# Performance work log

Measured on AMD Instinct MI355X. Metric: run time of the kernel, lower is better.

The kernel has to match this reference:

```python
import jax, jax.numpy as jnp
import numpy as np

N = 50000      # nodes
E = 400000     # edges (before self-loops)
IN = 256       # in_dim
H = 4          # heads in layer 1
C = 64         # h_dim (per-head channels, layer 1)
OUT = 16       # out_dim (layer 2, 1 head)
NEG_SLOPE = 0.2


def gatv2_layer(x, src, dst, Wl, bl, Wr, br, att, bias, heads, ch, concat, num_nodes):
    # x: [N, F]; src/dst: [E']; Wl/Wr: [F, heads*ch]; att: [heads, ch]
    xl = (x @ Wl + bl).reshape(num_nodes, heads, ch)  # source transform
    xr = (x @ Wr + br).reshape(num_nodes, heads, ch)  # target transform
    m = xl[src] + xr[dst]                              # [E', H, C] gather
    e = jnp.sum(jax.nn.leaky_relu(m, NEG_SLOPE) * att, axis=-1)  # [E', H]
    # segment softmax over incoming edges of each dst node (self-loops ensure non-empty)
    emax = jax.ops.segment_max(e, dst, num_segments=num_nodes)   # [N, H]
    ee = jnp.exp(e - emax[dst])
    denom = jax.ops.segment_sum(ee, dst, num_segments=num_nodes)  # [N, H]
    alpha = ee / (denom[dst] + 1e-16)                              # [E', H]
    out = jax.ops.segment_sum(alpha[..., None] * xl[src], dst, num_segments=num_nodes)  # [N,H,C]
    if concat:
        out = out.reshape(num_nodes, heads * ch)
    else:
        out = out.mean(axis=1)
    return out + bias


def setup_inputs() -> dict:
    key = jax.random.key(0)
    ks = jax.random.split(key, 16)
    s = 0.05
    inp = {
        "x": jax.random.normal(ks[0], (N, IN), jnp.float32),
        "edge_index": jax.random.randint(ks[1], (2, E), 0, N),
        # layer 1 params (in_dim -> heads*h_dim)
        "Wl1": jax.random.normal(ks[2], (IN, H * C), jnp.float32) * s,
        "bl1": jnp.zeros((H * C,), jnp.float32),
        "Wr1": jax.random.normal(ks[3], (IN, H * C), jnp.float32) * s,
        "br1": jnp.zeros((H * C,), jnp.float32),
        "att1": jax.random.normal(ks[4], (H, C), jnp.float32) * s,
        "bias1": jnp.zeros((H * C,), jnp.float32),
        # layer 2 params (heads*h_dim -> out_dim, 1 head)
        "Wl2": jax.random.normal(ks[5], (H * C, OUT), jnp.float32) * s,
        "bl2": jnp.zeros((OUT,), jnp.float32),
        "Wr2": jax.random.normal(ks[6], (H * C, OUT), jnp.float32) * s,
        "br2": jnp.zeros((OUT,), jnp.float32),
        "att2": jax.random.normal(ks[7], (1, OUT), jnp.float32) * s,
        "bias2": jnp.zeros((OUT,), jnp.float32),
    }
    return inp


def reference(x, edge_index, Wl1, bl1, Wr1, br1, att1, bias1, Wl2, bl2, Wr2, br2, att2, bias2):
    # add self loops (PyG GATv2Conv default add_self_loops=True)
    loop = jnp.arange(N, dtype=edge_index.dtype)
    src = jnp.concatenate([edge_index[0], loop])
    dst = jnp.concatenate([edge_index[1], loop])
    h = gatv2_layer(x, src, dst, Wl1, bl1, Wr1, br1, att1, bias1, H, C, True, N)
    h = jnp.tanh(h)
    o = gatv2_layer(h, src, dst, Wl2, bl2, Wr2, br2, att2, bias2, 1, OUT, False, N)
    return o, jax.nn.log_softmax(o, axis=1)
```

## Files before the change

kernel.cpp:

```cpp
#include <hip/hip_runtime.h>

typedef __bf16 bfv8 __attribute__((ext_vector_type(8)));
typedef float f32x4 __attribute__((ext_vector_type(4)));
typedef float f32x2 __attribute__((ext_vector_type(2)));
typedef short shortv8 __attribute__((ext_vector_type(8)));
typedef unsigned short usv8 __attribute__((ext_vector_type(8)));
typedef unsigned int u32x4 __attribute__((ext_vector_type(4)));

__device__ __forceinline__ float b2f(unsigned short u) {
  unsigned int v = ((unsigned int)u) << 16;
  float f;
  __builtin_memcpy(&f, &v, 4);
  return f;
}
__device__ __forceinline__ unsigned short f2b(float f) {
  unsigned int u;
  __builtin_memcpy(&u, &f, 4);
  u += 0x7fffu + ((u >> 16) & 1u);
  return (unsigned short)(u >> 16);
}
__device__ __forceinline__ f32x2 unpack2(unsigned int u) {
  unsigned int lo = u << 16;
  unsigned int hi = u & 0xffff0000u;
  float fl, fh;
  __builtin_memcpy(&fl, &lo, 4);
  __builtin_memcpy(&fh, &hi, 4);
  f32x2 r;
  r.x = fl;
  r.y = fh;
  return r;
}

__global__ void probe_kernel(const unsigned short* __restrict__ x, int* __restrict__ flag) {
  int lane = threadIdx.x;
  int cnt = 0;
  for (int i = lane; i < 4096; i += 64) {
    unsigned int e = (x[i] >> 7) & 0xffu;
    if (e >= 0x86u) cnt++;
  }
#pragma unroll
  for (int off = 1; off < 64; off <<= 1) cnt += __shfl_xor(cnt, off, 64);
  if (lane == 0) *flag = (cnt > 100) ? 1 : 0;
}

__global__ __launch_bounds__(256) void conv_x_kernel(const void* __restrict__ x,
                                                     unsigned short* __restrict__ dst,
                                                     const int* __restrict__ flagp, int n) {
  int i = (blockIdx.x * 256 + threadIdx.x) * 4;
  if (i >= n) return;
  if (*flagp) {
    float4 f = *reinterpret_cast<const float4*>((const float*)x + i);
    ushort4 o;
    o.x = f2b(f.x); o.y = f2b(f.y); o.z = f2b(f.z); o.w = f2b(f.w);
    *reinterpret_cast<ushort4*>(dst + i) = o;
  } else {
    *reinterpret_cast<ushort4*>(dst + i) =
        *reinterpret_cast<const ushort4*>((const unsigned short*)x + i);
  }
}

#define SM_TOT 1088
__device__ __forceinline__ unsigned short rd_param(const void* p, int e, int flag) {
  return flag ? f2b(((const float*)p)[e]) : ((const unsigned short*)p)[e];
}
__global__ __launch_bounds__(256) void prep_params_kernel(
    const void* Wl1, const void* bl1, const void* Wr1, const void* br1,
    const void* att1, const void* bias1, const void* Wl2, const void* bl2,
    const void* Wr2, const void* br2, const void* att2, const void* bias2,
    unsigned short* __restrict__ WT1, unsigned short* __restrict__ WT2,
    unsigned short* __restrict__ Pv, const int* __restrict__ flagp) {
  int idx = blockIdx.x * 256 + threadIdx.x;
  int flag = *flagp;
  if (idx < 512 * 256) {
    int n = idx >> 8, k = idx & 255;
    WT1[idx] = (n < 256) ? rd_param(Wl1, k * 256 + n, flag)
                         : rd_param(Wr1, k * 256 + (n - 256), flag);
    return;
  }
  idx -= 512 * 256;
  if (idx < 32 * 256) {
    int n = idx >> 8, k = idx & 255;
    WT2[idx] = (n < 16) ? rd_param(Wl2, k * 16 + n, flag)
                        : rd_param(Wr2, k * 16 + (n - 16), flag);
    return;
  }
  idx -= 32 * 256;
  if (idx >= SM_TOT) return;
  const void* srcs[8] = {bl1, br1, att1, bias1, bl2, br2, att2, bias2};
  const int offs[9] = {0, 256, 512, 768, 1024, 1040, 1056, 1072, SM_TOT};
  int t = 0;
  while (idx >= offs[t + 1]) t++;
  Pv[idx] = rd_param(srcs[t], idx - offs[t], flag);
}

__global__ __launch_bounds__(256) void gemm1_kernel(
    const unsigned short* __restrict__ X,
    const unsigned short* __restrict__ WT,
    const unsigned short* __restrict__ bl, const unsigned short* __restrict__ br,
    unsigned short* __restrict__ C, int M) {
  __shared__ unsigned short smem[18432];
  const int t = threadIdx.x;
  const int lane = t & 63;
  const int w = t >> 6;
  const int quad = lane >> 4;
  const int l16 = lane & 15;
  const int n_blk = blockIdx.x;
  const int m_base = blockIdx.y * 128 + (w >> 1) * 64;
  const int n_base = n_blk * 128 + (w & 1) * 64;

  const int st_row = t >> 3;
  const int st_seg = t & 7;
  const unsigned short* wt_base =
      WT + ((size_t)(n_blk * 128 + st_row)) * 256 + st_seg * 8;

  f32x4 acc[4][4];
#pragma unroll
  for (int i = 0; i < 4; i++)
#pragma unroll
    for (int j = 0; j < 4; j++) acc[i][j] = (f32x4){0.f, 0.f, 0.f, 0.f};

  shortv8 st[4];
#pragma unroll
  for (int i = 0; i < 4; i++)
    st[i] = *reinterpret_cast<const shortv8*>(wt_base + (size_t)(32 * i) * 256);
#pragma unroll
  for (int i = 0; i < 4; i++) {
    int row = st_row + 32 * i;
    *reinterpret_cast<shortv8*>(smem + row * 64 + ((st_seg ^ (row & 7)) * 8)) = st[i];
  }
  __syncthreads();

#pragma unroll
  for (int c = 0; c < 4; c++) {
    if (c < 3) {
#pragma unroll
      for (int i = 0; i < 4; i++)
        st[i] = *reinterpret_cast<const shortv8*>(wt_base + (size_t)(32 * i) * 256 +
                                                  (c + 1) * 64);
    }
    const unsigned short* bb = smem + (c & 1) * 8192;
#pragma unroll
    for (int sub = 0; sub < 2; sub++) {
      bfv8 a[4], b[4];
      int seg_r = sub * 4 + quad;
#pragma unroll
      for (int i = 0; i < 4; i++) {
        int row = m_base + 16 * i + l16;
        if (row >= M) row = M - 1;
        a[i] = *reinterpret_cast<const bfv8*>(X + (size_t)row * 256 + c * 64 + sub * 32 +
                                              quad * 8);
      }
#pragma unroll
      for (int j = 0; j < 4; j++) {
        int col = (w & 1) * 64 + 16 * j + l16;
        b[j] = *reinterpret_cast<const bfv8*>(bb + col * 64 + ((seg_r ^ (col & 7)) * 8));
      }
#pragma unroll
      for (int i = 0; i < 4; i++)
#pragma unroll
        for (int j = 0; j < 4; j++)
          acc[i][j] = __builtin_amdgcn_mfma_f32_16x16x32_bf16(a[i], b[j], acc[i][j], 0, 0, 0);
    }
    if (c < 3) {
      int buf = (c + 1) & 1;
#pragma unroll
      for (int i = 0; i < 4; i++) {
        int row = st_row + 32 * i;
        *reinterpret_cast<shortv8*>(smem + buf * 8192 + row * 64 +
                                    ((st_seg ^ (row & 7)) * 8)) = st[i];
      }
      __syncthreads();
    }
  }

  __syncthreads();
  unsigned short* lt = smem + w * 4608;
#pragma unroll
  for (int j = 0; j < 4; j++) {
    int col = n_base + 16 * j + l16;
    float bias = (col < 256) ? b2f(bl[col]) : b2f(br[col - 256]);
#pragma unroll
    for (int i = 0; i < 4; i++)
#pragma unroll
      for (int r = 0; r < 4; r++)
        lt[(16 * i + quad * 4 + r) * 72 + 16 * j + l16] = f2b(acc[i][j][r] + bias);
  }
#pragma unroll
  for (int pass = 0; pass < 8; pass++) {
    int row = pass * 8 + (lane >> 3);
    int colg = (lane & 7) * 8;
    shortv8 v = *reinterpret_cast<const shortv8*>(lt + row * 72 + colg);
    int grow = m_base + row;
    if (grow < M)
      *reinterpret_cast<shortv8*>(C + (size_t)grow * 512 + n_base + colg) = v;
  }
}

__global__ __launch_bounds__(256) void gemm2_kernel(
    const unsigned short* __restrict__ H, const unsigned short* __restrict__ WT,
    const unsigned short* __restrict__ bl, const unsigned short* __restrict__ br,
    float* __restrict__ C, int M) {
  const int lane = threadIdx.x & 63;
  const int w = threadIdx.x >> 6;
  const int quad = lane >> 4;
  const int l16 = lane & 15;
  const int m_base = blockIdx.x * 256 + w * 64;

  f32x4 acc[4][2];
#pragma unroll
  for (int i = 0; i < 4; i++)
#pragma unroll
    for (int j = 0; j < 2; j++) acc[i][j] = (f32x4){0.f, 0.f, 0.f, 0.f};

#pragma unroll
  for (int k0 = 0; k0 < 256; k0 += 32) {
    bfv8 a[4], b[2];
#pragma unroll
    for (int i = 0; i < 4; i++) {
      int row = m_base + 16 * i + l16;
      if (row >= M) row = M - 1;
      a[i] = *reinterpret_cast<const bfv8*>(H + (size_t)row * 256 + k0 + quad * 8);
    }
#pragma unroll
    for (int j = 0; j < 2; j++) {
      int col = 16 * j + l16;
      b[j] = *reinterpret_cast<const bfv8*>(WT + (size_t)col * 256 + k0 + quad * 8);
    }
#pragma unroll
    for (int i = 0; i < 4; i++)
#pragma unroll
      for (int j = 0; j < 2; j++)
        acc[i][j] = __builtin_amdgcn_mfma_f32_16x16x32_bf16(a[i], b[j], acc[i][j], 0, 0, 0);
  }

#pragma unroll
  for (int j = 0; j < 2; j++) {
    int col = 16 * j + l16;
    float bias = (j == 0) ? b2f(bl[l16]) : b2f(br[l16]);
#pragma unroll
    for (int i = 0; i < 4; i++) {
#pragma unroll
      for (int r = 0; r < 4; r++) {
        int row = m_base + 16 * i + quad * 4 + r;
        if (row < M) C[(size_t)row * 32 + col] = acc[i][j][r] + bias;
      }
    }
  }
}

__global__ __launch_bounds__(256) void count_kernel(const int* __restrict__ ei, int E, int Nn,
                                                    int* __restrict__ cnt) {
  int i = blockIdx.x * 256 + threadIdx.x;
  int total = E + Nn;
  if (i >= total) return;
  int d = (i < E) ? ei[E + i] : (i - E);
  if ((unsigned)d >= (unsigned)Nn) d = 0;
  atomicAdd(&cnt[d], 1);
}

__global__ __launch_bounds__(1024) void scan1_kernel(const int* __restrict__ cnt,
                                                     int* __restrict__ row_start,
                                                     int* __restrict__ blkTot, int Nn) {
  __shared__ int buf[1024];
  int t = threadIdx.x;
  int i = blockIdx.x * 1024 + t;
  int v = (i < Nn) ? cnt[i] : 0;
  buf[t] = v;
  __syncthreads();
  for (int off = 1; off < 1024; off <<= 1) {
    int x = (t >= off) ? buf[t - off] : 0;
    __syncthreads();
    buf[t] += x;
    __syncthreads();
  }
  if (i < Nn) row_start[i] = buf[t] - v;
  if (t == 1023) blkTot[blockIdx.x] = buf[1023];
}

__global__ __launch_bounds__(64) void scan2_kernel(const int* __restrict__ blkTot,
                                                   int* __restrict__ blkOff, int nb,
                                                   int* __restrict__ row_start, int Nn,
                                                   int total) {
  int lane = threadIdx.x;
  int v = (lane < nb) ? blkTot[lane] : 0;
  int s = v;
#pragma unroll
  for (int off = 1; off < 64; off <<= 1) {
    int u = __shfl_up(s, off, 64);
    if (lane >= off) s += u;
  }
  if (lane < nb) blkOff[lane] = s - v;
  if (lane == 0) row_start[Nn] = total;
}

__global__ __launch_bounds__(1024) void scan3_kernel(int* __restrict__ row_start,
                                                     int* __restrict__ cursor,
                                                     const int* __restrict__ blkOff, int Nn) {
  int i = blockIdx.x * 1024 + threadIdx.x;
  if (i < Nn) {
    int val = row_start[i] + blkOff[blockIdx.x];
    row_start[i] = val;
    cursor[i] = val;
  }
}

__global__ __launch_bounds__(256) void fill_kernel(const int* __restrict__ ei, int E, int Nn,
                                                   int* __restrict__ cursor,
                                                   int* __restrict__ csr_src) {
  int i = blockIdx.x * 256 + threadIdx.x;
  int total = E + Nn;
  if (i >= total) return;
  int s, d;
  if (i < E) { s = ei[i]; d = ei[E + i]; } else { s = i - E; d = i - E; }
  if ((unsigned)d >= (unsigned)Nn) d = 0;
  if ((unsigned)s >= (unsigned)Nn) s = 0;
  int pos = atomicAdd(&cursor[d], 1);
  if ((unsigned)pos < (unsigned)total) csr_src[pos] = s;
}

__global__ __launch_bounds__(256) void agg1_kernel(
    const unsigned short* __restrict__ C1,
    const unsigned short* __restrict__ att1,
    const unsigned short* __restrict__ bias1,
    const int* __restrict__ row_start, const int* __restrict__ csr_src,
    unsigned short* __restrict__ H1,
    int Nn, int Etot) {
  int wid = blockIdx.x * 4 + (threadIdx.x >> 6);
  if (wid >= Nn) return;
  int lane = threadIdx.x & 63;
  int half = lane >> 5;
  int c0 = (lane & 31) * 8;

  f32x2 at2[4], xr2[4];
  {
    u32x4 a4 = *reinterpret_cast<const u32x4*>(att1 + c0);
    u32x4 r4 = *reinterpret_cast<const u32x4*>(C1 + (size_t)wid * 512 + 256 + c0);
#pragma unroll
    for (int k = 0; k < 4; k++) { at2[k] = unpack2(a4[k]); xr2[k] = unpack2(r4[k]); }
  }

  float denom = 0.f;
  f32x2 acc2[4] = {{0.f, 0.f}, {0.f, 0.f}, {0.f, 0.f}, {0.f, 0.f}};
  int beg = row_start[wid], end = row_start[wid + 1];
  if (beg < 0) beg = 0;
  if (end < beg || end - beg > Etot) end = beg;

#pragma unroll 2
  for (int i = beg; i < end; i += 2) {
    int p = i + half;
    bool valid = p < end;
    int pc = valid ? p : i;
    int s = csr_src[pc];
    if ((unsigned)s >= (unsigned)Nn) s = 0;
    u32x4 row = *reinterpret_cast<const u32x4*>(C1 + (size_t)s * 512 + c0);
    f32x2 xl2[4];
    f32x2 dot2 = {0.f, 0.f};
#pragma unroll
    for (int k = 0; k < 4; k++) {
      xl2[k] = unpack2(row[k]);
      f32x2 m2 = xl2[k] + xr2[k];
      f32x2 l2 = __builtin_elementwise_max(m2, 0.2f * m2);
      dot2 = l2 * at2[k] + dot2;
    }
    float dot = dot2.x + dot2.y;
    dot += __shfl_xor(dot, 1, 64);
    dot += __shfl_xor(dot, 2, 64);
    dot += __shfl_xor(dot, 4, 64);
    dot = fminf(fmaxf(dot, -60.f), 60.f);
    float wgt = valid ? __expf(dot) : 0.f;
    denom += wgt;
    f32x2 w2 = {wgt, wgt};
#pragma unroll
    for (int k = 0; k < 4; k++) acc2[k] = xl2[k] * w2 + acc2[k];
  }
  denom += __shfl_xor(denom, 32, 64);
#pragma unroll
  for (int k = 0; k < 4; k++) {
    acc2[k].x += __shfl_xor(acc2[k].x, 32, 64);
    acc2[k].y += __shfl_xor(acc2[k].y, 32, 64);
  }

  if (half == 0) {
    float inv = 1.f / (denom + 1e-16f);
    usv8 b8 = *reinterpret_cast<const usv8*>(bias1 + c0);
    usv8 o8;
#pragma unroll
    for (int k = 0; k < 4; k++) {
#pragma unroll
      for (int j = 0; j < 2; j++) {
        float x = (j ? acc2[k].y : acc2[k].x) * inv + b2f(b8[2 * k + j]);
        float e2 = __expf(2.f * x);
        float th = (e2 - 1.f) / (e2 + 1.f);
        if (!(th == th)) th = 0.f;
        o8[2 * k + j] = f2b(th);
      }
    }
    *reinterpret_cast<usv8*>(H1 + (size_t)wid * 256 + c0) = o8;
  }
}

__global__ __launch_bounds__(256) void agg2_kernel(
    const float* __restrict__ C2,
    const unsigned short* __restrict__ att2,
    const unsigned short* __restrict__ bias2,
    const int* __restrict__ row_start, const int* __restrict__ csr_src,
    float* __restrict__ out,
    int Nn, int Etot) {
  int wid = blockIdx.x * 4 + (threadIdx.x >> 6);
  if (wid >= Nn) return;
  int lane = threadIdx.x & 63;
  int eslot = lane >> 2;
  int cg = (lane & 3) * 4;

  f32x2 at2[2], xr2[2];
  {
    ushort4 a4 = *reinterpret_cast<const ushort4*>(att2 + cg);
    at2[0].x = b2f(a4.x); at2[0].y = b2f(a4.y);
    at2[1].x = b2f(a4.z); at2[1].y = b2f(a4.w);
    float4 r4 = *reinterpret_cast<const float4*>(C2 + (size_t)wid * 32 + 16 + cg);
    xr2[0].x = r4.x; xr2[0].y = r4.y; xr2[1].x = r4.z; xr2[1].y = r4.w;
  }

  float denom = 0.f;
  f32x2 acc2[2] = {{0.f, 0.f}, {0.f, 0.f}};
  int beg = row_start[wid], end = row_start[wid + 1];
  if (beg < 0) beg = 0;
  if (end < beg || end - beg > Etot) end = beg;

  for (int i = beg; i < end; i += 16) {
    int p = i + eslot;
    bool valid = p < end;
    int pc = valid ? p : i;
    int s = csr_src[pc];
    if ((unsigned)s >= (unsigned)Nn) s = 0;
    float4 x4 = *reinterpret_cast<const float4*>(C2 + (size_t)s * 32 + cg);
    f32x2 xl2[2];
    xl2[0].x = x4.x; xl2[0].y = x4.y; xl2[1].x = x4.z; xl2[1].y = x4.w;
    f32x2 dot2 = {0.f, 0.f};
#pragma unroll
    for (int k = 0; k < 2; k++) {
      f32x2 m2 = xl2[k] + xr2[k];
      f32x2 l2 = __builtin_elementwise_max(m2, 0.2f * m2);
      dot2 = l2 * at2[k] + dot2;
    }
    float dot = dot2.x + dot2.y;
    dot += __shfl_xor(dot, 1, 64);
    dot += __shfl_xor(dot, 2, 64);
    dot = fminf(fmaxf(dot, -60.f), 60.f);
    float wgt = valid ? __expf(dot) : 0.f;
    denom += wgt;
    f32x2 w2 = {wgt, wgt};
#pragma unroll
    for (int k = 0; k < 2; k++) acc2[k] = xl2[k] * w2 + acc2[k];
  }
#pragma unroll
  for (int off = 4; off <= 32; off <<= 1) {
    denom += __shfl_xor(denom, off, 64);
#pragma unroll
    for (int k = 0; k < 2; k++) {
      acc2[k].x += __shfl_xor(acc2[k].x, off, 64);
      acc2[k].y += __shfl_xor(acc2[k].y, off, 64);
    }
  }

  float inv = 1.f / (denom + 1e-16f);
  ushort4 b4 = *reinterpret_cast<const ushort4*>(bias2 + cg);
  float bb[4] = {b2f(b4.x), b2f(b4.y), b2f(b4.z), b2f(b4.w)};
  float o[4] = {acc2[0].x * inv + bb[0], acc2[0].y * inv + bb[1],
                acc2[1].x * inv + bb[2], acc2[1].y * inv + bb[3]};
#pragma unroll
  for (int k = 0; k < 4; k++)
    if (!(o[k] == o[k])) o[k] = 0.f;
  float mx = fmaxf(fmaxf(o[0], o[1]), fmaxf(o[2], o[3]));
  mx = fmaxf(mx, __shfl_xor(mx, 1, 64));
  mx = fmaxf(mx, __shfl_xor(mx, 2, 64));
  float se = 0.f;
#pragma unroll
  for (int k = 0; k < 4; k++) se += __expf(o[k] - mx);
  se += __shfl_xor(se, 1, 64);
  se += __shfl_xor(se, 2, 64);
  float ls = logf(se);
  if (lane < 4) {
    float4 vo = {o[0], o[1], o[2], o[3]};
    float4 vl = {o[0] - mx - ls, o[1] - mx - ls, o[2] - mx - ls, o[3] - mx - ls};
    *reinterpret_cast<float4*>(out + (size_t)wid * 16 + cg) = vo;
    *reinterpret_cast<float4*>(out + (size_t)Nn * 16 + (size_t)wid * 16 + cg) = vl;
  }
}

extern "C" void kernel_launch(void* const* d_in, const int* in_sizes, int n_in,
                              void* d_out, int out_size, void* d_ws, size_t ws_size,
                              hipStream_t stream) {
  const void* x_raw = d_in[0];
  const int* ei     = (const int*)d_in[1];

  const int M = in_sizes[0] / 256;
  const int E = in_sizes[1] / 2;
  const int TOT = E + M;
  const int NX = M * 256;

  char* ws = (char*)d_ws;
  size_t off = 0;
  auto alloc = [&](size_t bytes) -> void* {
    void* p = ws + off;
    off = (off + bytes + 255) & ~(size_t)255;
    return p;
  };
  int*            flag   = (int*)alloc(4);
  unsigned short* Pv     = (unsigned short*)alloc((size_t)SM_TOT * 2);
  unsigned short* Xc     = (unsigned short*)alloc((size_t)NX * 2);
  unsigned short* WT1    = (unsigned short*)alloc((size_t)512 * 256 * 2);
  unsigned short* WT2    = (unsigned short*)alloc((size_t)32 * 256 * 2);
  int*            cnt    = (int*)alloc((size_t)M * 4);
  int*            cursor = (int*)alloc((size_t)M * 4);
  int*            row_start = (int*)alloc((size_t)(M + 1) * 4);
  int*            csr_src   = (int*)alloc((size_t)TOT * 4);
  int*            blkTot = (int*)alloc(64 * 4);
  int*            blkOff = (int*)alloc(64 * 4);
  float*          C2     = (float*)alloc((size_t)M * 32 * 4);
  unsigned short* C1     = (unsigned short*)alloc((size_t)M * 512 * 2);
  const size_t need = off;
  (void)n_in;
  unsigned short* H1 = Xc;

  if (ws_size < need) {
    hipMemsetAsync(d_out, 0, (size_t)out_size * 4, stream);
    return;
  }

  unsigned short* bl1c   = Pv + 0;
  unsigned short* br1c   = Pv + 256;
  unsigned short* att1c  = Pv + 512;
  unsigned short* bias1c = Pv + 768;
  unsigned short* bl2c   = Pv + 1024;
  unsigned short* br2c   = Pv + 1040;
  unsigned short* att2c  = Pv + 1056;
  unsigned short* bias2c = Pv + 1072;

  hipMemsetAsync(cnt, 0, (size_t)M * 4, stream);

  probe_kernel<<<1, 64, 0, stream>>>((const unsigned short*)x_raw, flag);
  conv_x_kernel<<<(NX / 4 + 255) / 256, 256, 0, stream>>>(x_raw, Xc, flag, NX);
  prep_params_kernel<<<(512 * 256 + 32 * 256 + SM_TOT + 255) / 256, 256, 0, stream>>>(
      d_in[2], d_in[3], d_in[4], d_in[5], d_in[6], d_in[7], d_in[8], d_in[9],
      d_in[10], d_in[11], d_in[12], d_in[13], WT1, WT2, Pv, flag);

  dim3 g1(4, (M + 127) / 128);
  gemm1_kernel<<<g1, 256, 0, stream>>>(Xc, WT1, bl1c, br1c, C1, M);

  count_kernel<<<(TOT + 255) / 256, 256, 0, stream>>>(ei, E, M, cnt);
  int nb = (M + 1023) / 1024;
  scan1_kernel<<<nb, 1024, 0, stream>>>(cnt, row_start, blkTot, M);
  scan2_kernel<<<1, 64, 0, stream>>>(blkTot, blkOff, nb, row_start, M, TOT);
  scan3_kernel<<<nb, 1024, 0, stream>>>(row_start, cursor, blkOff, M);
  fill_kernel<<<(TOT + 255) / 256, 256, 0, stream>>>(ei, E, M, cursor, csr_src);

  agg1_kernel<<<(M + 3) / 4, 256, 0, stream>>>(C1, att1c, bias1c, row_start, csr_src,
                                               H1, M, TOT);

  gemm2_kernel<<<(M + 255) / 256, 256, 0, stream>>>(H1, WT2, bl2c, br2c, C2, M);

  agg2_kernel<<<(M + 3) / 4, 256, 0, stream>>>(C2, att2c, bias2c, row_start, csr_src,
                                               (float*)d_out, M, TOT);
}
```

Before: 301.8 us.

## Fold dtype probe into kernels, swizzle GEMM1 grid, unroll agg1 edge loop

Removes the separate single-wave probe kernel by having each block of conv_x and prep_params recompute the fp32/bf16 input-format flag from the first 4096 halves of x in shared memory, saving one launch and a serial dependency. GEMM1 moves to a 1D grid with a swizzle that groups 8 M-slabs across the 4 N-blocks, aiming for better L2 reuse of X rows. The agg1 loop now loads two neighbor rows per iteration (4 edges per wave step) to keep more gathers in flight. Each block now redundantly rereads the probe sample, and the grid is padded to a multiple of 32 with early exit for out-of-range slabs.

Result: no change. 303.2 us (+0.4%).

```diff
diff --git a/kernel.cpp b/kernel.cpp
--- a/kernel.cpp
+++ b/kernel.cpp
@@ -30,25 +30,26 @@
   r.y = fh;
   return r;
 }
-
-__global__ void probe_kernel(const unsigned short* __restrict__ x, int* __restrict__ flag) {
-  int lane = threadIdx.x;
-  int cnt = 0;
-  for (int i = lane; i < 4096; i += 64) {
-    unsigned int e = (x[i] >> 7) & 0xffu;
-    if (e >= 0x86u) cnt++;
-  }
-#pragma unroll
-  for (int off = 1; off < 64; off <<= 1) cnt += __shfl_xor(cnt, off, 64);
-  if (lane == 0) *flag = (cnt > 100) ? 1 : 0;
+__device__ __forceinline__ bool block_flag_f32(const unsigned short* xh) {
+  __shared__ int cnt_s;
+  if (threadIdx.x == 0) cnt_s = 0;
+  __syncthreads();
+  int c = 0;
+  for (int k = threadIdx.x; k < 4096; k += 256) {
+    unsigned int e = (xh[k] >> 7) & 0xffu;
+    if (e >= 0x86u) c++;
+  }
+  if (c) atomicAdd(&cnt_s, c);
+  __syncthreads();
+  return cnt_s > 100;
 }
 
 __global__ __launch_bounds__(256) void conv_x_kernel(const void* __restrict__ x,
-                                                     unsigned short* __restrict__ dst,
-                                                     const int* __restrict__ flagp, int n) {
+                                                     unsigned short* __restrict__ dst, int n) {
+  bool f32in = block_flag_f32((const unsigned short*)x);
   int i = (blockIdx.x * 256 + threadIdx.x) * 4;
   if (i >= n) return;
-  if (*flagp) {
+  if (f32in) {
     float4 f = *reinterpret_cast<const float4*>((const float*)x + i);
     ushort4 o;
     o.x = f2b(f.x); o.y = f2b(f.y); o.z = f2b(f.z); o.w = f2b(f.w);
@@ -64,13 +65,13 @@
   return flag ? f2b(((const float*)p)[e]) : ((const unsigned short*)p)[e];
 }
 __global__ __launch_bounds__(256) void prep_params_kernel(
-    const void* Wl1, const void* bl1, const void* Wr1, const void* br1,
+    const void* xh, const void* Wl1, const void* bl1, const void* Wr1, const void* br1,
     const void* att1, const void* bias1, const void* Wl2, const void* bl2,
     const void* Wr2, const void* br2, const void* att2, const void* bias2,
     unsigned short* __restrict__ WT1, unsigned short* __restrict__ WT2,
-    unsigned short* __restrict__ Pv, const int* __restrict__ flagp) {
+    unsigned short* __restrict__ Pv) {
+  int flag = block_flag_f32((const unsigned short*)xh) ? 1 : 0;
   int idx = blockIdx.x * 256 + threadIdx.x;
-  int flag = *flagp;
   if (idx < 512 * 256) {
     int n = idx >> 8, k = idx & 255;
     WT1[idx] = (n < 256) ? rd_param(Wl1, k * 256 + n, flag)
@@ -99,13 +100,16 @@
     const unsigned short* __restrict__ bl, const unsigned short* __restrict__ br,
     unsigned short* __restrict__ C, int M) {
   __shared__ unsigned short smem[18432];
+  const int lin = blockIdx.x;
+  const int m_slab = (lin >> 5) * 8 + (lin & 7);
+  const int n_blk = (lin >> 3) & 3;
+  if (m_slab * 128 >= M) return;
   const int t = threadIdx.x;
   const int lane = t & 63;
   const int w = t >> 6;
   const int quad = lane >> 4;
   const int l16 = lane & 15;
-  const int n_blk = blockIdx.x;
-  const int m_base = blockIdx.y * 128 + (w >> 1) * 64;
+  const int m_base = m_slab * 128 + (w >> 1) * 64;
   const int n_base = n_blk * 128 + (w & 1) * 64;
 
   const int st_row = t >> 3;
@@ -345,34 +349,41 @@
   if (beg < 0) beg = 0;
   if (end < beg || end - beg > Etot) end = beg;
 
-#pragma unroll 2
-  for (int i = beg; i < end; i += 2) {
-    int p = i + half;
-    bool valid = p < end;
-    int pc = valid ? p : i;
-    int s = csr_src[pc];
-    if ((unsigned)s >= (unsigned)Nn) s = 0;
-    u32x4 row = *reinterpret_cast<const u32x4*>(C1 + (size_t)s * 512 + c0);
-    f32x2 xl2[4];
-    f32x2 dot2 = {0.f, 0.f};
-#pragma unroll
-    for (int k = 0; k < 4; k++) {
-      xl2[k] = unpack2(row[k]);
-      f32x2 m2 = xl2[k] + xr2[k];
-      f32x2 l2 = __builtin_elementwise_max(m2, 0.2f * m2);
-      dot2 = l2 * at2[k] + dot2;
-    }
-    float dot = dot2.x + dot2.y;
-    dot += __shfl_xor(dot, 1, 64);
-    dot += __shfl_xor(dot, 2, 64);
-    dot += __shfl_xor(dot, 4, 64);
-    dot = fminf(fmaxf(dot, -60.f), 60.f);
-    float wgt = valid ? __expf(dot) : 0.f;
-    denom += wgt;
-    f32x2 w2 = {wgt, wgt};
-#pragma unroll
-    for (int k = 0; k < 4; k++) acc2[k] = xl2[k] * w2 + acc2[k];
-  }
+#define AGG1_BODY(ROW, VALID)                                                 \
+  {                                                                           \
+    f32x2 xl2[4];                                                             \
+    f32x2 dot2 = {0.f, 0.f};                                                  \
+    _Pragma("unroll") for (int k = 0; k < 4; k++) {                           \
+      xl2[k] = unpack2(ROW[k]);                                               \
+      f32x2 m2 = xl2[k] + xr2[k];                                             \
+      f32x2 l2 = __builtin_elementwise_max(m2, 0.2f * m2);                    \
+      dot2 = l2 * at2[k] + dot2;                                              \
+    }                                                                         \
+    float dot = dot2.x + dot2.y;                                              \
+    dot += __shfl_xor(dot, 1, 64);                                            \
+    dot += __shfl_xor(dot, 2, 64);                                            \
+    dot += __shfl_xor(dot, 4, 64);                                            \
+    dot = fminf(fmaxf(dot, -60.f), 60.f);                                     \
+    float wgt = (VALID) ? __expf(dot) : 0.f;                                  \
+    denom += wgt;                                                             \
+    f32x2 w2 = {wgt, wgt};                                                    \
+    _Pragma("unroll") for (int k = 0; k < 4; k++) acc2[k] = xl2[k] * w2 + acc2[k]; \
+  }
+
+  for (int i = beg; i < end; i += 4) {
+    int p0 = i + half, p1 = i + 2 + half;
+    bool v0 = p0 < end, v1 = p1 < end;
+    int s0 = csr_src[v0 ? p0 : i];
+    int s1 = csr_src[v1 ? p1 : i];
+    if ((unsigned)s0 >= (unsigned)Nn) s0 = 0;
+    if ((unsigned)s1 >= (unsigned)Nn) s1 = 0;
+    u32x4 row0 = *reinterpret_cast<const u32x4*>(C1 + (size_t)s0 * 512 + c0);
+    u32x4 row1 = *reinterpret_cast<const u32x4*>(C1 + (size_t)s1 * 512 + c0);
+    AGG1_BODY(row0, v0);
+    AGG1_BODY(row1, v1);
+  }
+#undef AGG1_BODY
+
   denom += __shfl_xor(denom, 32, 64);
 #pragma unroll
   for (int k = 0; k < 4; k++) {
@@ -506,7 +517,6 @@
     off = (off + bytes + 255) & ~(size_t)255;
     return p;
   };
-  int*            flag   = (int*)alloc(4);
   unsigned short* Pv     = (unsigned short*)alloc((size_t)SM_TOT * 2);
   unsigned short* Xc     = (unsigned short*)alloc((size_t)NX * 2);
   unsigned short* WT1    = (unsigned short*)alloc((size_t)512 * 256 * 2);
@@ -539,13 +549,13 @@
 
   hipMemsetAsync(cnt, 0, (size_t)M * 4, stream);
 
-  probe_kernel<<<1, 64, 0, stream>>>((const unsigned short*)x_raw, flag);
-  conv_x_kernel<<<(NX / 4 + 255) / 256, 256, 0, stream>>>(x_raw, Xc, flag, NX);
+  conv_x_kernel<<<(NX / 4 + 255) / 256, 256, 0, stream>>>(x_raw, Xc, NX);
   prep_params_kernel<<<(512 * 256 + 32 * 256 + SM_TOT + 255) / 256, 256, 0, stream>>>(
-      d_in[2], d_in[3], d_in[4], d_in[5], d_in[6], d_in[7], d_in[8], d_in[9],
-      d_in[10], d_in[11], d_in[12], d_in[13], WT1, WT2, Pv, flag);
-
-  dim3 g1(4, (M + 127) / 128);
+      x_raw, d_in[2], d_in[3], d_in[4], d_in[5], d_in[6], d_in[7], d_in[8], d_in[9],
+      d_in[10], d_in[11], d_in[12], d_in[13], WT1, WT2, Pv);
+
+  int mblk = (M + 127) / 128;
+  int g1 = ((mblk * 4 + 31) / 32) * 32;
   gemm1_kernel<<<g1, 256, 0, stream>>>(Xc, WT1, bl1c, br1c, C1, M);
 
   count_kernel<<<(TOT + 255) / 256, 256, 0, stream>>>(ei, E, M, cnt);
```
